# Performance work log

Measured on AMD Instinct MI355X. Metric: run time of the kernel, lower is better.

## Reference

```python
import jax, jax.numpy as jnp
import numpy as np

B, P, T, V, N, D = 16, 96, 128, 64, 16, 128


def setup_inputs() -> dict:
    key = jax.random.key(0)
    ks = jax.random.split(key, 9)
    s = 0.05  # weight scale for stability
    return {
        "queries": jax.random.normal(ks[0], (B, P, V, D), jnp.float32),
        "keys": jax.random.normal(ks[1], (B, T, V, D), jnp.float32),
        "var_ccc": jax.random.randint(ks[2], (B, V, N), 0, V),
        "Wq": jax.random.normal(ks[3], (D, D), jnp.float32) * s,
        "bq": jnp.zeros((D,), jnp.float32),
        "Wkv": jax.random.normal(ks[4], (D, D), jnp.float32) * s,
        "bkv": jnp.zeros((D,), jnp.float32),
        "Wout": jax.random.normal(ks[5], (D, D), jnp.float32) * s,
        "bout": jnp.zeros((D,), jnp.float32),
    }


def reference(queries, keys, var_ccc, Wq, bq, Wkv, bkv, Wout, bout):
    b, p, v, d = queries.shape
    scale = d ** -0.5
    # projections (nn.Linear: x @ W.T + b)
    q = queries @ Wq.T + bq                      # [B,P,V,D]
    k = keys @ Wkv.T + bkv                       # [B,T,V,D]
    k_last = k[:, -p:]                           # [B,P,V,D]
    # irregular gather of neighbor keys per (batch, variable)
    idx = var_ccc.reshape(b, -1)                 # [B, V*N]
    kc = jax.vmap(lambda kb, ib: kb[:, ib])(k_last, idx)  # [B,P,V*N,D]
    kc = kc.reshape(b, p, v, -1, d)              # [B,P,V,N,D] (keys == values)
    # tiny 1xN attention per (b,p,v)
    scores = jnp.einsum('bpvd,bpvnd->bpvn', q, kc) * scale
    attn = jax.nn.softmax(scores, axis=-1)       # dropout is identity in eval
    out = jnp.einsum('bpvn,bpvnd->bpvd', attn, kc)  # [B,P,V,D]
    res = jnp.concatenate([k[:, :-p], out], axis=1)  # [B,T,V,D]
    return res @ Wout.T + bout
```

## Files before the change

kernel.cpp:

```cpp
#include <hip/hip_runtime.h>

#define BB 16
#define PP 96
#define TT 128
#define VV 64
#define NN 16
#define DD 128
#define BPP (BB * PP)
#define NPASS (BB * 32)
#define SB 136
#define ST 72
#define SSF 68

typedef __bf16 bf16x8 __attribute__((ext_vector_type(8)));
typedef __bf16 bf16x4 __attribute__((ext_vector_type(4)));
typedef float  floatx4 __attribute__((ext_vector_type(4)));

#define MFMA16(a, b, c) __builtin_amdgcn_mfma_f32_16x16x32_bf16(a, b, c, 0, 0, 0)

__device__ __forceinline__ bf16x8 cvt8(float4 a, float4 b) {
    return bf16x8{(__bf16)a.x, (__bf16)a.y, (__bf16)a.z, (__bf16)a.w,
                  (__bf16)b.x, (__bf16)b.y, (__bf16)b.z, (__bf16)b.w};
}

__device__ __forceinline__ void loadA_g(const float* Xs, int lm, int lq, bf16x8 af[4]) {
    const float4* p = (const float4*)(Xs + lm * DD + lq * 8);
#pragma unroll
    for (int ks = 0; ks < 4; ++ks) af[ks] = cvt8(p[8 * ks], p[8 * ks + 1]);
}

__device__ __forceinline__ void loadA_l(const __bf16* As, int sa, int lm, int lq,
                                        bf16x8* af, int kblocks) {
#pragma unroll
    for (int ks = 0; ks < 4; ++ks) {
        if (ks >= kblocks) break;
        af[ks] = *(const bf16x8*)(As + lm * sa + lq * 8 + 32 * ks);
    }
}

__device__ __forceinline__ void mmB(const bf16x8* af, const __bf16* B, int sb,
                                    int lm, int lq, floatx4* acc, int nblocks, int kblocks) {
#pragma unroll
    for (int nb = 0; nb < 8; ++nb) {
        if (nb >= nblocks) break;
        acc[nb] = floatx4{0.f, 0.f, 0.f, 0.f};
#pragma unroll
        for (int ks = 0; ks < 4; ++ks) {
            if (ks >= kblocks) break;
            bf16x8 bf = *(const bf16x8*)(B + (nb * 16 + lm) * sb + lq * 8 + 32 * ks);
            acc[nb] = MFMA16(af[ks], bf, acc[nb]);
        }
    }
}

__global__ void prep(const float* __restrict__ Wq, const float* __restrict__ Wkv,
                     const float* __restrict__ Wout, const float* __restrict__ bkv,
                     const float* __restrict__ bout,
                     __bf16* __restrict__ Wb, float* __restrict__ bcomb) {
    int i = blockIdx.x, j = threadIdx.x;
    Wb[i * DD + j]         = (__bf16)Wq[i * DD + j];
    Wb[16384 + i * DD + j] = (__bf16)Wkv[i * DD + j];
    Wb[32768 + i * DD + j] = (__bf16)Wout[i * DD + j];
    float acc = 0.f;
    for (int k = 0; k < DD; ++k) acc += Wout[i * DD + k] * Wkv[k * DD + j];
    Wb[49152 + i * DD + j] = (__bf16)acc;
    if (i == 0) {
        float bs = bout[j];
        for (int k = 0; k < DD; ++k) bs += Wout[j * DD + k] * bkv[k];
        bcomb[j] = bs;
    }
}

__global__ __launch_bounds__(256, 3) void fused(
    const float* __restrict__ queries, const float* __restrict__ keys,
    const int* __restrict__ ccc, const __bf16* __restrict__ Wb,
    const float* __restrict__ bq, const float* __restrict__ bkv,
    const float* __restrict__ bout, const float* __restrict__ bcomb,
    float* __restrict__ out) {
    __shared__ __align__(16) char lds[53248];
    __bf16* R1    = (__bf16*)lds;
    __bf16* smKs  = (__bf16*)(lds + 17408);
    __bf16* smKsT = (__bf16*)(lds + 34816);
    __bf16* smA   = smKs;
    float*  smS   = (float*)lds;

    int bl = blockIdx.x, t = threadIdx.x;
    int w = t >> 6, L = t & 63, lm = L & 15, lq = L >> 4;

    bf16x8 af[4];
    floatx4 acc[8];

    if (bl >= BPP) {
        int pb = bl - BPP;
        int b = pb >> 5, wi = pb & 31;
        const float* Xs = keys + ((long)b * TT * VV + wi * 64 + w * 16) * DD;
        float* Yg = out + ((long)b * TT * VV + wi * 64) * DD;
        loadA_g(Xs, lm, lq, af);
        mmB(af, Wb + 49152, DD, lm, lq, acc, 8, 4);
#pragma unroll
        for (int nb = 0; nb < 8; ++nb) {
            float bv = bcomb[nb * 16 + lm];
#pragma unroll
            for (int r = 0; r < 4; ++r)
                Yg[(long)(w * 16 + lq * 4 + r) * DD + nb * 16 + lm] = acc[nb][r] + bv;
        }
        return;
    }

    int b = bl / PP, p = bl % PP;
    const float* Qg = queries + ((long)(b * PP + p) * VV) * DD;
    const float* Kg = keys + ((long)(b * TT + 32 + p) * VV) * DD;
    float* Yg = out + ((long)(b * TT + 32 + p) * VV) * DD;

    int se[NN];
    if (L < 16) {
        const int4* cp = (const int4*)(ccc + ((long)b * VV + w * 16 + L) * NN);
#pragma unroll
        for (int i = 0; i < 4; ++i) {
            int4 c4 = cp[i];
            se[4 * i] = c4.x; se[4 * i + 1] = c4.y;
            se[4 * i + 2] = c4.z; se[4 * i + 3] = c4.w;
        }
    }

    loadA_g(Qg + w * 16 * DD, lm, lq, af);
    mmB(af, Wb, DD, lm, lq, acc, 8, 4);
#pragma unroll
    for (int nb = 0; nb < 8; ++nb) {
        float bv = bq[nb * 16 + lm];
#pragma unroll
        for (int r = 0; r < 4; ++r)
            R1[(w * 16 + lq * 4 + r) * SB + nb * 16 + lm] = (__bf16)(acc[nb][r] + bv);
    }

    loadA_g(Kg + w * 16 * DD, lm, lq, af);
    mmB(af, Wb + 16384, DD, lm, lq, acc, 8, 4);
#pragma unroll
    for (int nb = 0; nb < 8; ++nb) {
        float bv = bkv[nb * 16 + lm];
        bf16x4 tp;
#pragma unroll
        for (int r = 0; r < 4; ++r) {
            float vv = acc[nb][r] + bv;
            smKs[(w * 16 + lq * 4 + r) * SB + nb * 16 + lm] = (__bf16)vv;
            tp[r] = (__bf16)vv;
        }
        *(bf16x4*)(smKsT + (nb * 16 + lm) * ST + w * 16 + lq * 4) = tp;
    }
    __syncthreads();

    loadA_l(R1 + w * 16 * SB, SB, lm, lq, af, 4);
    mmB(af, smKs, SB, lm, lq, acc, 4, 4);
#pragma unroll
    for (int nb = 0; nb < 4; ++nb)
#pragma unroll
        for (int r = 0; r < 4; ++r)
            smS[(w * 16 + lq * 4 + r) * SSF + nb * 16 + lm] = acc[nb][r];
    __syncthreads();

    {
        unsigned* za = (unsigned*)(smA + (w * 16) * ST);
        for (int i = L; i < 16 * ST / 2; i += 64) za[i] = 0u;
        if (L < 16) {
            int v = w * 16 + L;
            float sc[NN], mx = -1e30f;
#pragma unroll
            for (int n = 0; n < NN; ++n) {
                sc[n] = smS[v * SSF + se[n]] * 0.08838834764831845f;
                mx = fmaxf(mx, sc[n]);
            }
            float sum = 0.f;
#pragma unroll
            for (int n = 0; n < NN; ++n) { sc[n] = __expf(sc[n] - mx); sum += sc[n]; }
            float inv = 1.f / sum;
#pragma unroll
            for (int n = 0; n < NN; ++n) {
                int u = se[n];
                smA[v * ST + u] = (__bf16)((float)smA[v * ST + u] + sc[n] * inv);
            }
        }
    }

    loadA_l(smA + w * 16 * ST, ST, lm, lq, af, 2);
    mmB(af, smKsT, ST, lm, lq, acc, 8, 2);
#pragma unroll
    for (int nb = 0; nb < 8; ++nb)
#pragma unroll
        for (int r = 0; r < 4; ++r)
            R1[(w * 16 + lq * 4 + r) * SB + nb * 16 + lm] = (__bf16)acc[nb][r];

    loadA_l(R1 + w * 16 * SB, SB, lm, lq, af, 4);
    mmB(af, Wb + 32768, DD, lm, lq, acc, 8, 4);
#pragma unroll
    for (int nb = 0; nb < 8; ++nb) {
        float bv = bout[nb * 16 + lm];
#pragma unroll
        for (int r = 0; r < 4; ++r)
            Yg[(long)(w * 16 + lq * 4 + r) * DD + nb * 16 + lm] = acc[nb][r] + bv;
    }
}

extern "C" void kernel_launch(void* const* d_in, const int* in_sizes, int n_in,
                              void* d_out, int out_size, void* d_ws, size_t ws_size,
                              hipStream_t stream) {
    const float* queries = (const float*)d_in[0];
    const float* keys    = (const float*)d_in[1];
    const int*   ccc     = (const int*)d_in[2];
    const float* Wq      = (const float*)d_in[3];
    const float* bq      = (const float*)d_in[4];
    const float* Wkv     = (const float*)d_in[5];
    const float* bkv     = (const float*)d_in[6];
    const float* Wout    = (const float*)d_in[7];
    const float* bout    = (const float*)d_in[8];
    float* out = (float*)d_out;

    __bf16* Wb    = (__bf16*)d_ws;
    float*  bcomb = (float*)((char*)d_ws + 131072);

    prep<<<dim3(128), dim3(128), 0, stream>>>(Wq, Wkv, Wout, bkv, bout, Wb, bcomb);

    fused<<<dim3(BPP + NPASS), dim3(256), 0, stream>>>(
        queries, keys, ccc, Wb, bq, bkv, bout, bcomb, out);
}
```

Measured before the change: 252.7 us.

## Prefetch Q/K rows, spread softmax across all lanes, drop a block barrier

Q and K input rows are now loaded into registers up front, so both global loads are in flight before the first projection starts. The softmax and the scatter into the attention matrix now use all 64 lanes of each wave instead of 16. Duplicate neighbour indices are resolved by an equality-sum rather than read-modify-write. The attention matrix now lives in a per-wave slice of LDS that overlaps that wave's own score rows, which removes one __syncthreads. The costs are more register pressure from the prefetched data and redundant exp/sum work in every lane.

```diff
diff --git a/kernel.cpp b/kernel.cpp
--- a/kernel.cpp
+++ b/kernel.cpp
@@ -11,6 +11,8 @@
 #define SB 136
 #define ST 72
 #define SSF 68
+#define SCALE 0.08838834764831845f
+#define SLICE 4352
 
 typedef __bf16 bf16x8 __attribute__((ext_vector_type(8)));
 typedef __bf16 bf16x4 __attribute__((ext_vector_type(4)));
@@ -81,7 +83,6 @@
     __bf16* R1    = (__bf16*)lds;
     __bf16* smKs  = (__bf16*)(lds + 17408);
     __bf16* smKsT = (__bf16*)(lds + 34816);
-    __bf16* smA   = smKs;
     float*  smS   = (float*)lds;
 
     int bl = blockIdx.x, t = threadIdx.x;
@@ -112,9 +113,19 @@
     const float* Kg = keys + ((long)(b * TT + 32 + p) * VV) * DD;
     float* Yg = out + ((long)(b * TT + 32 + p) * VV) * DD;
 
+    float4 qr[8], kr[8];
+    {
+        const float4* qp = (const float4*)(Qg + (w * 16 + lm) * DD + lq * 8);
+        const float4* kp = (const float4*)(Kg + (w * 16 + lm) * DD + lq * 8);
+#pragma unroll
+        for (int ks = 0; ks < 4; ++ks) {
+            qr[2 * ks] = qp[8 * ks]; qr[2 * ks + 1] = qp[8 * ks + 1];
+            kr[2 * ks] = kp[8 * ks]; kr[2 * ks + 1] = kp[8 * ks + 1];
+        }
+    }
     int se[NN];
-    if (L < 16) {
-        const int4* cp = (const int4*)(ccc + ((long)b * VV + w * 16 + L) * NN);
+    {
+        const int4* cp = (const int4*)(ccc + ((long)b * VV + w * 16 + lm) * NN);
 #pragma unroll
         for (int i = 0; i < 4; ++i) {
             int4 c4 = cp[i];
@@ -123,7 +134,8 @@
         }
     }
 
-    loadA_g(Qg + w * 16 * DD, lm, lq, af);
+#pragma unroll
+    for (int ks = 0; ks < 4; ++ks) af[ks] = cvt8(qr[2 * ks], qr[2 * ks + 1]);
     mmB(af, Wb, DD, lm, lq, acc, 8, 4);
 #pragma unroll
     for (int nb = 0; nb < 8; ++nb) {
@@ -133,7 +145,8 @@
             R1[(w * 16 + lq * 4 + r) * SB + nb * 16 + lm] = (__bf16)(acc[nb][r] + bv);
     }
 
-    loadA_g(Kg + w * 16 * DD, lm, lq, af);
+#pragma unroll
+    for (int ks = 0; ks < 4; ++ks) af[ks] = cvt8(kr[2 * ks], kr[2 * ks + 1]);
     mmB(af, Wb + 16384, DD, lm, lq, acc, 8, 4);
 #pragma unroll
     for (int nb = 0; nb < 8; ++nb) {
@@ -156,32 +169,34 @@
 #pragma unroll
         for (int r = 0; r < 4; ++r)
             smS[(w * 16 + lq * 4 + r) * SSF + nb * 16 + lm] = acc[nb][r];
-    __syncthreads();
-
+
+    __bf16* smAsl = (__bf16*)(lds + w * SLICE);
     {
-        unsigned* za = (unsigned*)(smA + (w * 16) * ST);
+        int g = lq;
+        float sg[NN];
+        const float* Srow = smS + (w * 16 + lm) * SSF;
+#pragma unroll
+        for (int n = 0; n < NN; ++n) sg[n] = Srow[se[n]];
+        unsigned* za = (unsigned*)smAsl;
         for (int i = L; i < 16 * ST / 2; i += 64) za[i] = 0u;
-        if (L < 16) {
-            int v = w * 16 + L;
-            float sc[NN], mx = -1e30f;
-#pragma unroll
-            for (int n = 0; n < NN; ++n) {
-                sc[n] = smS[v * SSF + se[n]] * 0.08838834764831845f;
-                mx = fmaxf(mx, sc[n]);
-            }
-            float sum = 0.f;
-#pragma unroll
-            for (int n = 0; n < NN; ++n) { sc[n] = __expf(sc[n] - mx); sum += sc[n]; }
-            float inv = 1.f / sum;
-#pragma unroll
-            for (int n = 0; n < NN; ++n) {
-                int u = se[n];
-                smA[v * ST + u] = (__bf16)((float)smA[v * ST + u] + sc[n] * inv);
-            }
-        }
-    }
-
-    loadA_l(smA + w * 16 * ST, ST, lm, lq, af, 2);
+        float mx = -1e30f;
+#pragma unroll
+        for (int n = 0; n < NN; ++n) { sg[n] *= SCALE; mx = fmaxf(mx, sg[n]); }
+        float sum = 0.f;
+#pragma unroll
+        for (int n = 0; n < NN; ++n) { sg[n] = __expf(sg[n] - mx); sum += sg[n]; }
+        float inv = 1.f / sum;
+#pragma unroll
+        for (int j = 0; j < 4; ++j) {
+            int u = se[g * 4 + j];
+            float tot = 0.f;
+#pragma unroll
+            for (int n = 0; n < NN; ++n) tot += (se[n] == u) ? sg[n] : 0.f;
+            smAsl[lm * ST + u] = (__bf16)(tot * inv);
+        }
+    }
+
+    loadA_l(smAsl, ST, lm, lq, af, 2);
     mmB(af, smKsT, ST, lm, lq, acc, 8, 2);
 #pragma unroll
     for (int nb = 0; nb < 8; ++nb)
```

New measurement: 240.8 us. 4.7% less time.
